# Kernel tuning notes

Hardware: AMD Instinct MI355X
Metric: run time of the kernel (lower is better)

Reference implementation:

```python
import jax, jax.numpy as jnp
from jax import lax
import numpy as np

B, K = 32, 8
NUM_LABELS = 600
GRID = 100          # grid_size
FEATURE_DIM = 256
HUMAN = 100         # human_width == human_height


def setup_inputs() -> dict:
    rng = np.random.default_rng(0)
    ids = rng.integers(0, NUM_LABELS, size=(B, K))
    # Synthetic OA_distn: per-label MVN params (means + Cholesky factors of small covs).
    # Means chosen so sampled obj_x/obj_y are non-negative (well-defined slicing regime).
    mean_xy = rng.uniform(0.2, 0.8, size=(NUM_LABELS, 2)).astype(np.float32)
    mean_wh = rng.uniform(-0.3, 0.3, size=(NUM_LABELS, 2)).astype(np.float32)
    L = 0.05 * np.eye(2, dtype=np.float32)  # shared Cholesky factor (cov = L L^T)
    eps_xy = rng.standard_normal((B, K, 2)).astype(np.float32)
    eps_wh = rng.standard_normal((B, K, 2)).astype(np.float32)
    d_xy = mean_xy[ids] + eps_xy @ L.T      # MVN sample per (b,k): mean + L eps
    d_wh = mean_wh[ids] + eps_wh @ L.T
    delta_x, delta_y = d_xy[..., 0], d_xy[..., 1]
    delta_w, delta_h = d_wh[..., 0], d_wh[..., 1]
    # .int() truncation as in torch
    obj_x = np.clip((delta_x * HUMAN).astype(np.int32), 0, None)
    obj_y = np.clip((delta_y * HUMAN).astype(np.int32), 0, None)
    obj_w = (HUMAN * np.exp(delta_w)).astype(np.int32)
    obj_h = (HUMAN * np.exp(delta_h)).astype(np.int32)
    # global canvas size: host-side max, mirrors .max().item()
    g_w = int(np.maximum(HUMAN, obj_x + obj_w).max())
    g_h = int(np.maximum(HUMAN, obj_y + obj_h).max())
    # learned params
    ks = jax.random.split(jax.random.key(0), 3)
    conv1_w = jax.random.normal(ks[0], (16, 2, 3, 3), jnp.float32) * 0.1
    conv1_b = jnp.zeros((16,), jnp.float32)
    conv2_w = jax.random.normal(ks[1], (32, 16, 3, 3), jnp.float32) * 0.05
    conv2_b = jnp.zeros((32,), jnp.float32)
    proj_w = jax.random.normal(ks[2], (FEATURE_DIM, 32 * GRID * GRID), jnp.float32) * 0.002
    proj_b = jnp.zeros((FEATURE_DIM,), jnp.float32)
    return {
        'obj_x': jnp.asarray(obj_x), 'obj_y': jnp.asarray(obj_y),
        'obj_w': jnp.asarray(obj_w), 'obj_h': jnp.asarray(obj_h),
        'g_h': g_h, 'g_w': g_w,
        'conv1_w': conv1_w, 'conv1_b': conv1_b,
        'conv2_w': conv2_w, 'conv2_b': conv2_b,
        'proj_w': proj_w, 'proj_b': proj_b,
    }


def _binary_maps(obj_x, obj_y, obj_w, obj_h, g_h, g_w):
    # Vectorized rectangle rasterization on the (g_h, g_w) global canvas.
    b, k = obj_x.shape
    yy = jnp.arange(g_h)[None, None, :, None]   # (1,1,gH,1)
    xx = jnp.arange(g_w)[None, None, None, :]   # (1,1,1,gW)
    human = jnp.broadcast_to(((yy < HUMAN) & (xx < HUMAN)), (b, k, g_h, g_w)).astype(jnp.float32)
    ox = obj_x[..., None, None]; oy = obj_y[..., None, None]
    ow = obj_w[..., None, None]; oh = obj_h[..., None, None]
    obj = ((yy >= oy) & (yy < oy + oh) & (xx >= ox) & (xx < ox + ow)).astype(jnp.float32)
    maps = jnp.stack((human, obj), axis=2).reshape(b * k, 2, g_h, g_w)
    # bilinear, half-pixel centers, no antialias == torch F.interpolate(align_corners=False)
    return jax.image.resize(maps, (b * k, 2, GRID, GRID), method='bilinear', antialias=False)


def reference(obj_x, obj_y, obj_w, obj_h, g_h, g_w, conv1_w, conv1_b, conv2_w, conv2_b, proj_w, proj_b):
    b, k = obj_x.shape
    maps = _binary_maps(obj_x, obj_y, obj_w, obj_h, g_h, g_w)  # (B*K,2,GRID,GRID)
    dn = ('NCHW', 'OIHW', 'NCHW')
    x = lax.conv_general_dilated(maps, conv1_w, (1, 1), 'SAME', dimension_numbers=dn) + conv1_b[None, :, None, None]
    x = lax.conv_general_dilated(x, conv2_w, (1, 1), 'SAME', dimension_numbers=dn) + conv2_b[None, :, None, None]
    x = x.reshape(b * k, -1)                     # (B*K, 32*GRID*GRID), CHW order
    out = x @ proj_w.T + proj_b                  # (B*K, FEATURE_DIM)
    return out.reshape(b, k, FEATURE_DIM)
```

## Files before the change

### kernel.cpp

```cpp
#include <hip/hip_runtime.h>
#include <cstddef>

#define NS 256
#define NF 256
#define NC1 16
#define NC2 32

__global__ __launch_bounds__(256) void k_prep(
    const int* __restrict__ obx, const int* __restrict__ oby,
    const int* __restrict__ obw, const int* __restrict__ obh,
    const int* __restrict__ ghp, const int* __restrict__ gwp,
    const float* __restrict__ w1, const float* __restrict__ w2,
    const float* __restrict__ pb,
    float* __restrict__ pyT, float* __restrict__ pxT,
    float* __restrict__ hy, float* __restrict__ hx,
    float* __restrict__ Weff, float* __restrict__ base) {
  int tid = threadIdx.x;
  if (blockIdx.x == 0) {
    int n = tid;
    float gh = (float)ghp[0], gw = (float)gwp[0];
    float sy = gh / 100.0f, sx = gw / 100.0f;
    int x0 = obx[n], y0 = oby[n], w = obw[n], h = obh[n];
    for (int j = 0; j < 100; ++j) {
      float u = (j + 0.5f) * sx - 0.5f;
      int a0 = (int)floorf(u);
      float t = u - (float)a0;
      float v0 = (a0 >= x0 && a0 < x0 + w) ? 1.f : 0.f;
      float v1 = (a0 + 1 >= x0 && a0 + 1 < x0 + w) ? 1.f : 0.f;
      pxT[j * 256 + n] = (1.f - t) * v0 + t * v1;
      u = (j + 0.5f) * sy - 0.5f;
      a0 = (int)floorf(u);
      t = u - (float)a0;
      v0 = (a0 >= y0 && a0 < y0 + h) ? 1.f : 0.f;
      v1 = (a0 + 1 >= y0 && a0 + 1 < y0 + h) ? 1.f : 0.f;
      pyT[j * 256 + n] = (1.f - t) * v0 + t * v1;
    }
    if (n < 100) {
      int j = n;
      float u = (j + 0.5f) * sx - 0.5f;
      int a0 = (int)floorf(u);
      float t = u - (float)a0;
      float v0 = (a0 >= 0 && a0 < 100) ? 1.f : 0.f;
      float v1 = (a0 + 1 >= 0 && a0 + 1 < 100) ? 1.f : 0.f;
      hx[j] = (1.f - t) * v0 + t * v1;
      u = (j + 0.5f) * sy - 0.5f;
      a0 = (int)floorf(u);
      t = u - (float)a0;
      v0 = (a0 >= 0 && a0 < 100) ? 1.f : 0.f;
      v1 = (a0 + 1 >= 0 && a0 + 1 < 100) ? 1.f : 0.f;
      hy[j] = (1.f - t) * v0 + t * v1;
    }
  } else if (blockIdx.x == 1) {
    for (int idx = tid; idx < NC2 * 25; idx += 256) {
      int c2 = idx / 25, d = idx % 25;
      int dy = d / 5, dx = d % 5;
      float s = 0.f;
      for (int c1 = 0; c1 < NC1; ++c1)
        for (int sy = 0; sy < 3; ++sy) {
          int ty = dy - sy;
          if (ty < 0 || ty > 2) continue;
          for (int sx = 0; sx < 3; ++sx) {
            int tx = dx - sx;
            if (tx < 0 || tx > 2) continue;
            s += w1[((c1 * 2 + 1) * 3 + (2 - sy)) * 3 + (2 - sx)] *
                 w2[((c2 * NC1 + c1) * 9 + (2 - ty) * 3 + (2 - tx))];
          }
        }
      Weff[idx] = s;
    }
  } else {
    base[tid] = pb[tid];
  }
}

__global__ __launch_bounds__(256) void k_t2h(
    const float* __restrict__ w1, const float* __restrict__ b1,
    const float* __restrict__ w2, const float* __restrict__ b2,
    const float* __restrict__ hy, const float* __restrict__ hx,
    float* __restrict__ t2h) {
  __shared__ float t1s[NC1 * 3 * 104];
  __shared__ float hxs[104];
  __shared__ float hys[8];
  int tid = threadIdx.x;
  int row0 = blockIdx.x;
  int c2 = blockIdx.y * 8 + (tid >> 5);
  int colg = tid & 31;

  if (tid < 104) {
    int c = tid - 2;
    hxs[tid] = (c >= 0 && c < 100) ? hx[c] : 0.f;
  }
  if (tid >= 104 && tid < 109) {
    int d = tid - 104;
    int r = row0 - 2 + d;
    hys[d] = (r >= 0 && r < 100) ? hy[r] : 0.f;
  }
  __syncthreads();
  for (int i = tid; i < NC1 * 3 * 104; i += 256) {
    int c1 = i / 312, rem = i - c1 * 312;
    int r = rem / 104, j = rem - r * 104;
    int yy = row0 + r - 1, jc = j - 1;
    float val = 0.f;
    if (yy >= 0 && yy < 100 && jc >= 0 && jc < 100) {
      val = b1[c1];
#pragma unroll
      for (int dy = 0; dy < 3; ++dy) {
        float hv = hys[r + dy];
#pragma unroll
        for (int dx = 0; dx < 3; ++dx)
          val += w1[((c1 * 2 + 0) * 3 + dy) * 3 + dx] * hv * hxs[j + dx];
      }
    }
    t1s[i] = val;
  }
  __syncthreads();
  if (colg < 25) {
    float acc[4];
    float bb = b2[c2];
#pragma unroll
    for (int cc = 0; cc < 4; ++cc) acc[cc] = bb;
    for (int c1 = 0; c1 < NC1; ++c1)
#pragma unroll
      for (int r = 0; r < 3; ++r) {
        const float* tp = &t1s[(c1 * 3 + r) * 104 + colg * 4];
        float t0 = tp[0], t1 = tp[1], t2 = tp[2], t3 = tp[3], t4 = tp[4],
              t5 = tp[5];
#pragma unroll
        for (int dx = 0; dx < 3; ++dx) {
          float wv = w2[(c2 * NC1 + c1) * 9 + r * 3 + dx];
          float tv[6] = {t0, t1, t2, t3, t4, t5};
#pragma unroll
          for (int cc = 0; cc < 4; ++cc) acc[cc] += wv * tv[cc + dx];
        }
      }
    *(float4*)&t2h[c2 * 10000 + row0 * 100 + colg * 4] =
        make_float4(acc[0], acc[1], acc[2], acc[3]);
  }
}

__global__ __launch_bounds__(256) void k_adj5(
    const float* __restrict__ P, const float* __restrict__ Weff,
    const float* __restrict__ t2h, float* __restrict__ G,
    float* __restrict__ base, float* __restrict__ rimbuf) {
  __shared__ __align__(16) float buf[2][44 * 112];
  int tid = threadIdx.x;
  int f = blockIdx.y;
  int r0 = blockIdx.x * 40;
  const float* Pf = P + (size_t)f * (NC2 * 10000);
  float* rimf = rimbuf + (size_t)f * (NC2 * 400);

  auto stage = [&](float* b, int c2) {
    const float* Pc = Pf + c2 * 10000;
    float* rimc = rimf + c2 * 400;
    for (int w = tid; w < 44 * 32; w += 256) {
      int row = w >> 5, k = w & 31;
      int gr = r0 - 2 + row;
      if (k < 25 && gr >= 0 && gr < 100) {
        float4 val = *(const float4*)(Pc + gr * 100 + k * 4);
        *(float4*)(b + row * 112 + 4 + k * 4) = val;
        if (gr == 0) *(float4*)(rimc + k * 4) = val;
        if (gr == 99) *(float4*)(rimc + 100 + k * 4) = val;
        if (k == 0) rimc[200 + gr] = val.x;
        if (k == 24) rimc[300 + gr] = val.w;
      }
    }
  };

  for (int i = tid; i < 2 * 44 * 112; i += 256) ((float*)buf)[i] = 0.f;
  __syncthreads();
  stage(buf[0], 0);

  int colg = tid & 31, rowg = tid >> 5;
  bool act = (colg < 25) && (r0 + rowg * 5 < 100);
  float acc[5][4] = {};
  float bacc = 0.f;

  for (int c2 = 0; c2 < NC2; ++c2) {
    __syncthreads();
    if (c2 + 1 < NC2) stage(buf[(c2 + 1) & 1], c2 + 1);
    if (act) {
      const float* lp = &buf[c2 & 1][(rowg * 5) * 112 + colg * 4];
      const float* We = Weff + c2 * 25;
#pragma unroll
      for (int ir = 0; ir < 9; ++ir) {
        float4 A = *(const float4*)(lp + ir * 112);
        float4 Bv = *(const float4*)(lp + ir * 112 + 4);
        float4 Cv = *(const float4*)(lp + ir * 112 + 8);
        float v[12] = {A.x,  A.y,  A.z,  A.w,  Bv.x, Bv.y,
                       Bv.z, Bv.w, Cv.x, Cv.y, Cv.z, Cv.w};
#pragma unroll
        for (int rr = 0; rr < 5; ++rr) {
          int dy = ir - rr;
          if (dy < 0 || dy > 4) continue;
#pragma unroll
          for (int dx = 0; dx < 5; ++dx) {
            float w = We[dy * 5 + dx];
#pragma unroll
            for (int cc = 0; cc < 4; ++cc) acc[rr][cc] += w * v[2 + dx + cc];
          }
          if (dy == 2) {
            int grow = r0 + rowg * 5 + rr;
            float4 t =
                *(const float4*)(t2h + c2 * 10000 + grow * 100 + colg * 4);
            bacc += t.x * v[4] + t.y * v[5] + t.z * v[6] + t.w * v[7];
          }
        }
      }
    }
  }
  if (act) {
#pragma unroll
    for (int rr = 0; rr < 5; ++rr) {
      int grow = r0 + rowg * 5 + rr;
      *(float4*)&G[(size_t)f * 10000 + grow * 100 + colg * 4] =
          *(float4*)&acc[rr][0];
    }
  }
  __syncthreads();
  float* red = &buf[0][0];
  red[tid] = bacc;
  __syncthreads();
  for (int s = 128; s > 0; s >>= 1) {
    if (tid < s) red[tid] += red[tid + s];
    __syncthreads();
  }
  if (tid == 0) atomicAdd(&base[f], red[0]);
}

__global__ __launch_bounds__(256) void k_rim(
    const float* __restrict__ rimbuf, const float* __restrict__ w2,
    const float* __restrict__ w1, float* __restrict__ G) {
  __shared__ float rs[NC2 * 400];
  __shared__ float hs[NC1 * 404];
  __shared__ float w1s[288];
  int tid = threadIdx.x;
  int f = blockIdx.x;
  for (int i = tid; i < NC2 * 400; i += 256)
    rs[i] = rimbuf[(size_t)f * (NC2 * 400) + i];
  for (int i = tid; i < 288; i += 256) w1s[i] = w1[i];
  __syncthreads();
  for (int qq = 0; qq < 2; ++qq) {
    int j = tid + qq * 256;
    if (j >= 404) break;
    int qy, qx;
    if (j < 102) { qy = -1; qx = j - 1; }
    else if (j < 204) { qy = 100; qx = j - 103; }
    else if (j < 304) { qy = j - 204; qx = -1; }
    else { qy = j - 304; qx = 100; }
    float hacc[NC1];
#pragma unroll
    for (int c1 = 0; c1 < NC1; ++c1) hacc[c1] = 0.f;
#pragma unroll
    for (int ty = 0; ty < 3; ++ty)
#pragma unroll
      for (int tx = 0; tx < 3; ++tx) {
        int r = qy + ty - 1, c = qx + tx - 1;
        bool ok = (r >= 0 && r < 100 && c >= 0 && c < 100);
        int side, i2;
        if (r == 0) { side = 0; i2 = c; }
        else if (r == 99) { side = 1; i2 = c; }
        else if (c == 0) { side = 2; i2 = r; }
        else { side = 3; i2 = r; }
        i2 = min(max(i2, 0), 99);
        int rbase = side * 100 + i2;
        if (ok) {
          for (int c2 = 0; c2 < NC2; ++c2) {
            float val = rs[c2 * 400 + rbase];
#pragma unroll
            for (int c1 = 0; c1 < NC1; ++c1)
              hacc[c1] +=
                  w2[(c2 * NC1 + c1) * 9 + (2 - ty) * 3 + (2 - tx)] * val;
          }
        }
      }
#pragma unroll
    for (int c1 = 0; c1 < NC1; ++c1) hs[c1 * 404 + j] = hacc[c1];
  }
  __syncthreads();
  for (int idx = tid; idx < 396; idx += 256) {
    int py, px;
    if (idx < 100) { py = 0; px = idx; }
    else if (idx < 200) { py = 99; px = idx - 100; }
    else if (idx < 298) { py = idx - 199; px = 0; }
    else { py = idx - 297; px = 99; }
    float corr = 0.f;
    for (int sy = 0; sy < 3; ++sy)
      for (int sx = 0; sx < 3; ++sx) {
        int qy = py + sy - 1, qx = px + sx - 1;
        bool ph = (qy == -1 || qy == 100 || qx == -1 || qx == 100);
        if (!ph) continue;
        int j;
        if (qy == -1) j = qx + 1;
        else if (qy == 100) j = 103 + qx;
        else if (qx == -1) j = 204 + qy;
        else j = 304 + qy;
#pragma unroll
        for (int c1 = 0; c1 < NC1; ++c1)
          corr += w1s[((c1 * 2 + 1) * 3 + (2 - sy)) * 3 + (2 - sx)] *
                  hs[c1 * 404 + j];
      }
    G[(size_t)f * 10000 + py * 100 + px] -= corr;
  }
}

__global__ __launch_bounds__(256) void k_gemm(
    const float* __restrict__ G, const float* __restrict__ pyT,
    const float* __restrict__ pxT, float* __restrict__ part) {
  __shared__ float Gs[8 * 132];
  __shared__ float Ms[8 * 128];
  int tid = threadIdx.x;
  int fT = blockIdx.x, nT = blockIdx.y, kS = blockIdx.z;
  int f0 = fT * 128, n0 = nT * 128, kb0 = kS * 80;
  int tf = tid % 16, tn = tid / 16;
  int fG = tid >> 1, kq = (tid & 1) * 4;
  int nl = tid & 127, kh = tid >> 7;
  float acc[8][8] = {};
  for (int ch = 0; ch < 10; ++ch) {
    int kb = kb0 + ch * 8;
    __syncthreads();
    {
      float4 g = *(const float4*)&G[(size_t)(f0 + fG) * 10000 + kb + kq];
      Gs[(kq + 0) * 132 + fG] = g.x;
      Gs[(kq + 1) * 132 + fG] = g.y;
      Gs[(kq + 2) * 132 + fG] = g.z;
      Gs[(kq + 3) * 132 + fG] = g.w;
    }
#pragma unroll
    for (int kk = 0; kk < 4; ++kk) {
      int k = kh * 4 + kk;
      int p = kb + k;
      int pi = p / 100, pj = p - pi * 100;
      Ms[k * 128 + nl] = pyT[pi * 256 + n0 + nl] * pxT[pj * 256 + n0 + nl];
    }
    __syncthreads();
#pragma unroll
    for (int k = 0; k < 8; ++k) {
      float4 ga = *(const float4*)&Gs[k * 132 + tf * 4];
      float4 gb = *(const float4*)&Gs[k * 132 + 64 + tf * 4];
      float4 ma = *(const float4*)&Ms[k * 128 + tn * 8];
      float4 mb = *(const float4*)&Ms[k * 128 + tn * 8 + 4];
      float gv[8] = {ga.x, ga.y, ga.z, ga.w, gb.x, gb.y, gb.z, gb.w};
      float mv[8] = {ma.x, ma.y, ma.z, ma.w, mb.x, mb.y, mb.z, mb.w};
#pragma unroll
      for (int nn = 0; nn < 8; ++nn)
#pragma unroll
        for (int ff = 0; ff < 8; ++ff) acc[nn][ff] += mv[nn] * gv[ff];
    }
  }
  size_t pb = (((size_t)kS * 2 + nT) * 2 + fT) * 16384;
#pragma unroll
  for (int nn = 0; nn < 8; ++nn) {
    int row = tn * 8 + nn;
    *(float4*)&part[pb + row * 128 + tf * 4] =
        make_float4(acc[nn][0], acc[nn][1], acc[nn][2], acc[nn][3]);
    *(float4*)&part[pb + row * 128 + 64 + tf * 4] =
        make_float4(acc[nn][4], acc[nn][5], acc[nn][6], acc[nn][7]);
  }
}

__global__ __launch_bounds__(256) void k_out(
    const float* __restrict__ part, const float* __restrict__ base,
    float* __restrict__ out) {
  int gid = blockIdx.x * 256 + threadIdx.x;
  int f = gid & 255, n = gid >> 8;
  int nT = n >> 7, nl = n & 127, fT = f >> 7, fl = f & 127;
  float val = base[f];
  size_t off = ((size_t)(nT * 2 + fT)) * 16384 + nl * 128 + fl;
  for (int s = 0; s < 125; ++s) val += part[(size_t)s * 65536 + off];
  out[(size_t)n * 256 + f] = val;
}

extern "C" void kernel_launch(void* const* d_in, const int* in_sizes, int n_in,
                              void* d_out, int out_size, void* d_ws,
                              size_t ws_size, hipStream_t stream) {
  const int* obj_x = (const int*)d_in[0];
  const int* obj_y = (const int*)d_in[1];
  const int* obj_w = (const int*)d_in[2];
  const int* obj_h = (const int*)d_in[3];
  const int* g_h = (const int*)d_in[4];
  const int* g_w = (const int*)d_in[5];
  const float* conv1_w = (const float*)d_in[6];
  const float* conv1_b = (const float*)d_in[7];
  const float* conv2_w = (const float*)d_in[8];
  const float* conv2_b = (const float*)d_in[9];
  const float* proj_w = (const float*)d_in[10];
  const float* proj_b = (const float*)d_in[11];
  float* out = (float*)d_out;

  float* w = (float*)d_ws;
  float* pyT = w;    w += 100 * 256;
  float* pxT = w;    w += 100 * 256;
  float* hy = w;     w += 100;
  float* hx = w;     w += 100;
  float* t2h = w;    w += NC2 * 10000;
  float* base = w;   w += NF;
  float* Weff = w;   w += NC2 * 25;
  float* G = w;      w += (size_t)NF * 10000;
  float* rimbuf = w; w += (size_t)NF * NC2 * 400;
  float* part = w;   w += (size_t)500 * 16384;

  k_prep<<<3, 256, 0, stream>>>(obj_x, obj_y, obj_w, obj_h, g_h, g_w, conv1_w,
                                conv2_w, proj_b, pyT, pxT, hy, hx, Weff, base);
  k_t2h<<<dim3(100, 4), 256, 0, stream>>>(conv1_w, conv1_b, conv2_w, conv2_b,
                                          hy, hx, t2h);
  k_adj5<<<dim3(3, 256), 256, 0, stream>>>(proj_w, Weff, t2h, G, base, rimbuf);
  k_rim<<<256, 256, 0, stream>>>(rimbuf, conv2_w, conv1_w, G);
  k_gemm<<<dim3(2, 2, 125), 256, 0, stream>>>(G, pyT, pxT, part);
  k_out<<<256, 256, 0, stream>>>(part, base, out);
}
```

Baseline: 717.4 us.

## Load adjoint conv windows directly into registers and split final reduction in two

k_adj5 drops the double-buffered shared-memory staging of proj_w rows. Each thread now loads its 9x3 float4 window straight from global memory into registers, reads the 5x5 weights from a small shared table, and covers 50 rows per block with 250 of 256 threads active. The change removes per-channel __syncthreads and shared-memory traffic, at the cost of redundant overlapping global loads and higher register pressure. The final 125-way partial sum is also split into a parallel 5x25 stage plus a small 5-way stage, so the reduction runs across more blocks.

```diff
diff --git a/kernel.cpp b/kernel.cpp
--- a/kernel.cpp
+++ b/kernel.cpp
@@ -138,86 +138,87 @@
   }
 }
 
-__global__ __launch_bounds__(256) void k_adj5(
+__global__ __launch_bounds__(256, 2) void k_adj5(
     const float* __restrict__ P, const float* __restrict__ Weff,
     const float* __restrict__ t2h, float* __restrict__ G,
     float* __restrict__ base, float* __restrict__ rimbuf) {
-  __shared__ __align__(16) float buf[2][44 * 112];
+  __shared__ float WeS[NC2 * 25];
+  __shared__ float red[256];
   int tid = threadIdx.x;
   int f = blockIdx.y;
-  int r0 = blockIdx.x * 40;
+  int r0 = blockIdx.x * 50;
   const float* Pf = P + (size_t)f * (NC2 * 10000);
   float* rimf = rimbuf + (size_t)f * (NC2 * 400);
 
-  auto stage = [&](float* b, int c2) {
-    const float* Pc = Pf + c2 * 10000;
-    float* rimc = rimf + c2 * 400;
-    for (int w = tid; w < 44 * 32; w += 256) {
-      int row = w >> 5, k = w & 31;
-      int gr = r0 - 2 + row;
-      if (k < 25 && gr >= 0 && gr < 100) {
-        float4 val = *(const float4*)(Pc + gr * 100 + k * 4);
-        *(float4*)(b + row * 112 + 4 + k * 4) = val;
-        if (gr == 0) *(float4*)(rimc + k * 4) = val;
-        if (gr == 99) *(float4*)(rimc + 100 + k * 4) = val;
-        if (k == 0) rimc[200 + gr] = val.x;
-        if (k == 24) rimc[300 + gr] = val.w;
-      }
-    }
-  };
-
-  for (int i = tid; i < 2 * 44 * 112; i += 256) ((float*)buf)[i] = 0.f;
-  __syncthreads();
-  stage(buf[0], 0);
-
-  int colg = tid & 31, rowg = tid >> 5;
-  bool act = (colg < 25) && (r0 + rowg * 5 < 100);
+  for (int i = tid; i < NC2 * 25; i += 256) WeS[i] = Weff[i];
+  __syncthreads();
+
+  int rowg = tid / 25, colg = tid - rowg * 25;
+  bool act = tid < 250;
+  int rs = r0 + rowg * 5;
   float acc[5][4] = {};
   float bacc = 0.f;
 
-  for (int c2 = 0; c2 < NC2; ++c2) {
-    __syncthreads();
-    if (c2 + 1 < NC2) stage(buf[(c2 + 1) & 1], c2 + 1);
-    if (act) {
-      const float* lp = &buf[c2 & 1][(rowg * 5) * 112 + colg * 4];
-      const float* We = Weff + c2 * 25;
+  if (act) {
+    for (int c2 = 0; c2 < NC2; ++c2) {
+      const float* Pc = Pf + c2 * 10000;
+      const float* Tc = t2h + c2 * 10000;
+      float* rimc = rimf + c2 * 400;
+      float4 win[9][3];
 #pragma unroll
       for (int ir = 0; ir < 9; ++ir) {
-        float4 A = *(const float4*)(lp + ir * 112);
-        float4 Bv = *(const float4*)(lp + ir * 112 + 4);
-        float4 Cv = *(const float4*)(lp + ir * 112 + 8);
-        float v[12] = {A.x,  A.y,  A.z,  A.w,  Bv.x, Bv.y,
-                       Bv.z, Bv.w, Cv.x, Cv.y, Cv.z, Cv.w};
+        int gr = rs - 2 + ir;
+        bool rok = (gr >= 0 && gr < 100);
+#pragma unroll
+        for (int j = 0; j < 3; ++j) {
+          int cf = colg - 1 + j;
+          win[ir][j] = (rok && cf >= 0 && cf < 25)
+                           ? *(const float4*)(Pc + gr * 100 + cf * 4)
+                           : make_float4(0.f, 0.f, 0.f, 0.f);
+        }
+      }
+      float Wv[25];
+#pragma unroll
+      for (int i = 0; i < 25; ++i) Wv[i] = WeS[c2 * 25 + i];
+#pragma unroll
+      for (int ir = 0; ir < 9; ++ir) {
+        float v[12] = {win[ir][0].x, win[ir][0].y, win[ir][0].z, win[ir][0].w,
+                       win[ir][1].x, win[ir][1].y, win[ir][1].z, win[ir][1].w,
+                       win[ir][2].x, win[ir][2].y, win[ir][2].z, win[ir][2].w};
 #pragma unroll
         for (int rr = 0; rr < 5; ++rr) {
           int dy = ir - rr;
           if (dy < 0 || dy > 4) continue;
 #pragma unroll
           for (int dx = 0; dx < 5; ++dx) {
-            float w = We[dy * 5 + dx];
+            float w = Wv[dy * 5 + dx];
 #pragma unroll
             for (int cc = 0; cc < 4; ++cc) acc[rr][cc] += w * v[2 + dx + cc];
           }
-          if (dy == 2) {
-            int grow = r0 + rowg * 5 + rr;
-            float4 t =
-                *(const float4*)(t2h + c2 * 10000 + grow * 100 + colg * 4);
-            bacc += t.x * v[4] + t.y * v[5] + t.z * v[6] + t.w * v[7];
-          }
         }
       }
-    }
-  }
-  if (act) {
-#pragma unroll
-    for (int rr = 0; rr < 5; ++rr) {
-      int grow = r0 + rowg * 5 + rr;
-      *(float4*)&G[(size_t)f * 10000 + grow * 100 + colg * 4] =
-          *(float4*)&acc[rr][0];
-    }
-  }
-  __syncthreads();
-  float* red = &buf[0][0];
+#pragma unroll
+      for (int rr = 0; rr < 5; ++rr) {
+        float4 t = *(const float4*)(Tc + (rs + rr) * 100 + colg * 4);
+        float4 p = win[rr + 2][1];
+        bacc += t.x * p.x + t.y * p.y + t.z * p.z + t.w * p.w;
+      }
+      if (rs == 0) *(float4*)(rimc + colg * 4) = win[2][1];
+      if (rs == 95) *(float4*)(rimc + 100 + colg * 4) = win[6][1];
+      if (colg == 0) {
+#pragma unroll
+        for (int rr = 0; rr < 5; ++rr) rimc[200 + rs + rr] = win[rr + 2][1].x;
+      }
+      if (colg == 24) {
+#pragma unroll
+        for (int rr = 0; rr < 5; ++rr) rimc[300 + rs + rr] = win[rr + 2][1].w;
+      }
+    }
+#pragma unroll
+    for (int rr = 0; rr < 5; ++rr)
+      *(float4*)&G[(size_t)f * 10000 + (rs + rr) * 100 + colg * 4] =
+          make_float4(acc[rr][0], acc[rr][1], acc[rr][2], acc[rr][3]);
+  }
   red[tid] = bacc;
   __syncthreads();
   for (int s = 128; s > 0; s >>= 1) {
@@ -358,16 +359,28 @@
   }
 }
 
-__global__ __launch_bounds__(256) void k_out(
-    const float* __restrict__ part, const float* __restrict__ base,
+__global__ __launch_bounds__(256) void k_out1(
+    const float* __restrict__ part, float* __restrict__ part2) {
+  int gid = blockIdx.x * 256 + threadIdx.x;
+  int g = blockIdx.y;
+  int f = gid & 255, n = gid >> 8;
+  int nT = n >> 7, nl = n & 127, fT = f >> 7, fl = f & 127;
+  size_t off = ((size_t)(nT * 2 + fT)) * 16384 + nl * 128 + fl;
+  float val = 0.f;
+  for (int s = g * 25; s < g * 25 + 25; ++s)
+    val += part[(size_t)s * 65536 + off];
+  part2[(size_t)g * 65536 + gid] = val;
+}
+
+__global__ __launch_bounds__(256) void k_out2(
+    const float* __restrict__ part2, const float* __restrict__ base,
     float* __restrict__ out) {
   int gid = blockIdx.x * 256 + threadIdx.x;
-  int f = gid & 255, n = gid >> 8;
-  int nT = n >> 7, nl = n & 127, fT = f >> 7, fl = f & 127;
+  int f = gid & 255;
   float val = base[f];
-  size_t off = ((size_t)(nT * 2 + fT)) * 16384 + nl * 128 + fl;
-  for (int s = 0; s < 125; ++s) val += part[(size_t)s * 65536 + off];
-  out[(size_t)n * 256 + f] = val;
+#pragma unroll
+  for (int g = 0; g < 5; ++g) val += part2[(size_t)g * 65536 + gid];
+  out[gid] = val;
 }
 
 extern "C" void kernel_launch(void* const* d_in, const int* in_sizes, int n_in,
@@ -398,13 +411,15 @@
   float* G = w;      w += (size_t)NF * 10000;
   float* rimbuf = w; w += (size_t)NF * NC2 * 400;
   float* part = w;   w += (size_t)500 * 16384;
+  float* part2 = w;  w += (size_t)5 * 65536;
 
   k_prep<<<3, 256, 0, stream>>>(obj_x, obj_y, obj_w, obj_h, g_h, g_w, conv1_w,
                                 conv2_w, proj_b, pyT, pxT, hy, hx, Weff, base);
   k_t2h<<<dim3(100, 4), 256, 0, stream>>>(conv1_w, conv1_b, conv2_w, conv2_b,
                                           hy, hx, t2h);
-  k_adj5<<<dim3(3, 256), 256, 0, stream>>>(proj_w, Weff, t2h, G, base, rimbuf);
+  k_adj5<<<dim3(2, 256), 256, 0, stream>>>(proj_w, Weff, t2h, G, base, rimbuf);
   k_rim<<<256, 256, 0, stream>>>(rimbuf, conv2_w, conv1_w, G);
   k_gemm<<<dim3(2, 2, 125), 256, 0, stream>>>(G, pyT, pxT, part);
-  k_out<<<256, 256, 0, stream>>>(part, base, out);
-}
+  k_out1<<<dim3(256, 5), 256, 0, stream>>>(part, part2);
+  k_out2<<<256, 256, 0, stream>>>(part2, base, out);
+}
```

After: 682.7 us. 1.05x faster.
